# Kernel tuning notes

Hardware: AMD Instinct MI355X
Metric: run time of the kernel (lower is better)

The kernel has to match this reference:

```python
import jax, jax.numpy as jnp
import numpy as np

ALPHA = 16.0
K = 32
NUM_INSTANCES = 8  # samples per class in the batch (required by the original reshape logic)


def setup_inputs() -> dict:
    key = jax.random.key(0)
    n, d = 4096, 128
    inputs = jax.random.normal(key, (n, d), dtype=jnp.float32)
    # identity-sampler style labels: each class appears exactly NUM_INSTANCES times,
    # as assumed by the original pos_dist.resize(...) logic
    targets = (jnp.arange(n) // NUM_INSTANCES).astype(jnp.int64)
    return {"inputs": inputs, "targets": targets}


def reference(inputs, targets):
    n = inputs.shape[0]
    # L2-normalize rows (normalized=True)
    x = inputs / jnp.linalg.norm(inputs, axis=1, keepdims=True)
    # squared euclidean distance matrix: ||xi||^2 + ||xj||^2 - 2 xi.xj
    sq = jnp.sum(x * x, axis=1)  # [n]
    dist = sq[:, None] + sq[None, :] - 2.0 * (x @ x.T)  # [n, n]

    eye = jnp.eye(n, dtype=bool)
    same = targets[:, None] == targets[None, :]
    pos_mask = same & ~eye          # positives, excluding self
    neg_mask = ~same                # negatives

    inf = jnp.float32(jnp.inf)
    # threshold = K-th smallest (0-indexed) among the n-1 off-diagonal dists per row
    row_sorted = jnp.sort(jnp.where(eye, inf, dist), axis=1)
    thr = row_sorted[:, K]  # [n]

    base = jnp.mean(dist, axis=1, keepdims=True)  # mean over full row (incl. diagonal 0)
    below = dist < thr[:, None]
    pos_sel = pos_mask & below
    neg_sel = neg_mask & below

    expo = jnp.exp(ALPHA * (base - dist))  # [n, n]
    pos_logit = jnp.sum(jnp.where(pos_sel, expo, 0.0), axis=1)
    neg_logit = jnp.sum(jnp.where(neg_sel, expo, 0.0), axis=1)

    # fallback when no positive is below the threshold: use the closest positive
    min_pos = jnp.min(jnp.where(pos_mask, dist, inf), axis=1)
    fallback = jnp.exp(ALPHA * (base[:, 0] - min_pos))
    has_pos = jnp.any(pos_sel, axis=1)
    pos_logit = jnp.where(has_pos, pos_logit, fallback)

    loss_i = -jnp.log(pos_logit / (pos_logit + neg_logit))  # [n]
    loss = jnp.mean(loss_i)
    accuracy = jnp.mean((loss_i < 0.6).astype(jnp.float32))
    pos_d = jnp.sum(jnp.where(pos_mask, dist, 0.0)) / jnp.sum(pos_mask)
    neg_d = jnp.sum(jnp.where(neg_mask, dist, 0.0)) / jnp.sum(neg_mask)
    return loss, accuracy, pos_d, neg_d
```

## Files before the change

### kernel.cpp

```cpp
#include <hip/hip_runtime.h>
#include <math.h>

#define N 4096
#define D 128
#define RPB 8
#define NT 512
#define KSEL 32
#define CAND 320
#define ALPHA_C 16.0f

__device__ inline float waveSumF(float v){
  #pragma unroll
  for (int o = 32; o; o >>= 1) v += __shfl_xor(v, o);
  return v;
}
__device__ inline int waveSumI(int v){
  #pragma unroll
  for (int o = 32; o; o >>= 1) v += __shfl_xor(v, o);
  return v;
}
__device__ inline float waveMinF(float v){
  #pragma unroll
  for (int o = 32; o; o >>= 1) v = fminf(v, __shfl_xor(v, o));
  return v;
}

__device__ inline unsigned fkey(float f){
  unsigned u = __float_as_uint(f);
  return u ^ ((u >> 31) ? 0xFFFFFFFFu : 0x80000000u);
}
__device__ inline float fkey_inv(unsigned u){
  unsigned bits = (u & 0x80000000u) ? (u ^ 0x80000000u) : ~u;
  return __uint_as_float(bits);
}

__global__ __launch_bounds__(256) void knorm(const float* __restrict__ in,
                                             float* __restrict__ xn,
                                             float* __restrict__ xnT,
                                             float* __restrict__ sq){
  int row = blockIdx.x * 4 + (threadIdx.x >> 6);
  int lane = threadIdx.x & 63;
  const float* p = in + (size_t)row * D;
  float e0 = p[lane], e1 = p[lane + 64];
  float s = waveSumF(e0*e0 + e1*e1);
  float inv = 1.0f / sqrtf(s);
  float x0 = e0 * inv, x1 = e1 * inv;
  float s2 = waveSumF(x0*x0 + x1*x1);
  xn[(size_t)row * D + lane]      = x0;
  xn[(size_t)row * D + lane + 64] = x1;
  xnT[(size_t)lane * N + row]        = x0;
  xnT[(size_t)(lane + 64) * N + row] = x1;
  if (lane == 0) sq[row] = s2;
}

__global__ __launch_bounds__(NT, 2) void kmain(const float* __restrict__ xn,
                                               const float* __restrict__ xnT,
                                               const float* __restrict__ sq,
                                               const int* __restrict__ tgt,
                                               double* __restrict__ accum){
  __shared__ float dist[RPB][N];
  __shared__ float xi[RPB][D];
  __shared__ float cand[RPB][CAND];
  __shared__ int   ccnt[RPB];
  __shared__ float scr2[8][RPB + 2];
  __shared__ float scr3[8][RPB];
  __shared__ float baseSh[RPB], minposSh[RPB], lsSh[RPB], acSh[RPB];

  const int tid  = threadIdx.x;
  const int lane = tid & 63;
  const int w    = tid >> 6;
  const int i0   = blockIdx.x * RPB;

  for (int t = tid; t < RPB * D; t += NT)
    (&xi[0][0])[t] = xn[(size_t)i0 * D + t];
  if (tid < RPB) ccnt[tid] = 0;
  __syncthreads();

  float sqi[RPB]; int ti[RPB];
  #pragma unroll
  for (int r = 0; r < RPB; ++r){ sqi[r] = sq[i0 + r]; ti[r] = tgt[i0 + r]; }

  const int jA = 512 * w + 4 * lane;
  const int jB = jA + 256;
  const float4* T4 = (const float4*)xnT;
  const int fA = 128 * w + lane;
  const int fB = fA + 64;

  float acc[RPB][8];
  #pragma unroll
  for (int r = 0; r < RPB; ++r)
    #pragma unroll
    for (int q = 0; q < 8; ++q) acc[r][q] = 0.f;

  for (int k = 0; k < D; ++k){
    float4 vA = T4[(size_t)k * (N/4) + fA];
    float4 vB = T4[(size_t)k * (N/4) + fB];
    float xik[RPB];
    #pragma unroll
    for (int r = 0; r < RPB; ++r) xik[r] = xi[r][k];
    #pragma unroll
    for (int r = 0; r < RPB; ++r){
      acc[r][0] += xik[r] * vA.x;  acc[r][1] += xik[r] * vA.y;
      acc[r][2] += xik[r] * vA.z;  acc[r][3] += xik[r] * vA.w;
      acc[r][4] += xik[r] * vB.x;  acc[r][5] += xik[r] * vB.y;
      acc[r][6] += xik[r] * vB.z;  acc[r][7] += xik[r] * vB.w;
    }
  }

  float4 sqA = ((const float4*)sq)[fA], sqB = ((const float4*)sq)[fB];
  int4   tgA = ((const int4*)tgt)[fA],  tgB = ((const int4*)tgt)[fB];
  float sqj[8] = {sqA.x,sqA.y,sqA.z,sqA.w, sqB.x,sqB.y,sqB.z,sqB.w};
  int   tj [8] = {tgA.x,tgA.y,tgA.z,tgA.w, tgB.x,tgB.y,tgB.z,tgB.w};

  float bsum[RPB], mpos[RPB];
  #pragma unroll
  for (int r = 0; r < RPB; ++r){ bsum[r] = 0.f; mpos[r] = INFINITY; }
  float posd = 0.f, negd = 0.f;

  #pragma unroll
  for (int r = 0; r < RPB; ++r){
    float dv[8];
    #pragma unroll
    for (int q = 0; q < 8; ++q){
      int j = (q < 4) ? (jA + q) : (jB + q - 4);
      float dj = sqi[r] + sqj[q] - 2.0f * acc[r][q];
      bsum[r] += dj;
      bool same = (tj[q] == ti[r]);
      bool diag = (j == i0 + r);
      if (same && !diag){ posd += dj; mpos[r] = fminf(mpos[r], dj); }
      if (!same) negd += dj;
      dv[q] = diag ? INFINITY : dj;
    }
    ((float4*)&dist[r][jA])[0] = make_float4(dv[0], dv[1], dv[2], dv[3]);
    ((float4*)&dist[r][jB])[0] = make_float4(dv[4], dv[5], dv[6], dv[7]);
  }

  #pragma unroll
  for (int r = 0; r < RPB; ++r){
    float v = waveSumF(bsum[r]); if (lane == 0) scr2[w][r] = v;
    float m = waveMinF(mpos[r]); if (lane == 0) scr3[w][r] = m;
  }
  { float v = waveSumF(posd); if (lane == 0) scr2[w][RPB]   = v; }
  { float v = waveSumF(negd); if (lane == 0) scr2[w][RPB+1] = v; }
  __syncthreads();
  if (tid < RPB){
    float s = 0.f, m = INFINITY;
    #pragma unroll
    for (int q = 0; q < 8; ++q){ s += scr2[q][tid]; m = fminf(m, scr3[q][tid]); }
    baseSh[tid]   = s * (1.0f / (float)N);
    minposSh[tid] = m;
  }
  if (tid == RPB){
    float s = 0.f;
    #pragma unroll
    for (int q = 0; q < 8; ++q) s += scr2[q][RPB];
    atomicAdd(&accum[2], (double)s);
  }
  if (tid == RPB + 1){
    float s = 0.f;
    #pragma unroll
    for (int q = 0; q < 8; ++q) s += scr2[q][RPB+1];
    atomicAdd(&accum[3], (double)s);
  }
  __syncthreads();

  {
    const float4* drow = (const float4*)dist[w];
    unsigned lo = fkey(-0.5f);
    unsigned hi = fkey(4.5f);
    float thr;
    int   c = 0;
    bool  collected = false;

    while (hi - lo > 1u){
      unsigned mid = lo + ((hi - lo) >> 1);
      float pv = fkey_inv(mid);
      int cc = 0;
      #pragma unroll
      for (int t = 0; t < 16; ++t){
        float4 v = drow[lane + 64*t];
        cc += (v.x < pv) + (v.y < pv) + (v.z < pv) + (v.w < pv);
      }
      cc = waveSumI(cc);
      if (cc < KSEL + 1) lo = mid;
      else { hi = mid; if (cc <= CAND){ collected = true; c = cc; break; } }
    }

    if (collected){
      float pv = fkey_inv(hi);
      #pragma unroll
      for (int t = 0; t < 16; ++t){
        float4 v = drow[lane + 64*t];
        if (v.x < pv){ int ix = atomicAdd(&ccnt[w],1); if (ix < CAND) cand[w][ix] = v.x; }
        if (v.y < pv){ int ix = atomicAdd(&ccnt[w],1); if (ix < CAND) cand[w][ix] = v.y; }
        if (v.z < pv){ int ix = atomicAdd(&ccnt[w],1); if (ix < CAND) cand[w][ix] = v.z; }
        if (v.w < pv){ int ix = atomicAdd(&ccnt[w],1); if (ix < CAND) cand[w][ix] = v.w; }
      }
      __threadfence_block();
      float my[5]; int nm = 0;
      for (int t = lane; t < c; t += 64) my[nm++] = cand[w][t];
      for (int m = 0; m < nm; ++m){
        int myidx = lane + 64*m;
        float v = my[m];
        int rank = 0;
        for (int q = 0; q < c; ++q){
          float cq = cand[w][q];
          rank += (cq < v) || (cq == v && q < myidx);
        }
        if (rank == KSEL) lsSh[w] = v;
      }
      __threadfence_block();
      thr = lsSh[w];
    } else {
      thr = fkey_inv(lo);
    }

    const float base = baseSh[w];
    const int   tw   = ti[w];
    float pls = 0.f, nls = 0.f; int pcnt = 0;
    #pragma unroll 4
    for (int t = 0; t < 16; ++t){
      float4 v = drow[lane + 64*t];
      int4 tg = ((const int4*)tgt)[lane + 64*t];
      if (v.x < thr){ float e = expf(ALPHA_C*(base - v.x)); if (tg.x == tw){ pls += e; pcnt++; } else nls += e; }
      if (v.y < thr){ float e = expf(ALPHA_C*(base - v.y)); if (tg.y == tw){ pls += e; pcnt++; } else nls += e; }
      if (v.z < thr){ float e = expf(ALPHA_C*(base - v.z)); if (tg.z == tw){ pls += e; pcnt++; } else nls += e; }
      if (v.w < thr){ float e = expf(ALPHA_C*(base - v.w)); if (tg.w == tw){ pls += e; pcnt++; } else nls += e; }
    }
    pls = waveSumF(pls); nls = waveSumF(nls); pcnt = waveSumI(pcnt);
    if (lane == 0){
      float plogit = (pcnt > 0) ? pls : expf(ALPHA_C*(base - minposSh[w]));
      float li = -logf(plogit / (plogit + nls));
      lsSh[w] = li;
      acSh[w] = (li < 0.6f) ? 1.f : 0.f;
    }
  }
  __syncthreads();
  if (tid == 0){
    float ls = 0.f, ac = 0.f;
    #pragma unroll
    for (int r = 0; r < RPB; ++r){ ls += lsSh[r]; ac += acSh[r]; }
    atomicAdd(&accum[0], (double)ls);
    atomicAdd(&accum[1], (double)ac);
  }
}

__global__ void kfinal(const double* __restrict__ accum, float* __restrict__ out){
  out[0] = (float)(accum[0] / (double)N);
  out[1] = (float)(accum[1] / (double)N);
  out[2] = (float)(accum[2] / ((double)N * 7.0));
  out[3] = (float)(accum[3] / ((double)N * (double)(N - 8)));
}

extern "C" void kernel_launch(void* const* d_in, const int* in_sizes, int n_in,
                              void* d_out, int out_size, void* d_ws, size_t ws_size,
                              hipStream_t stream){
  (void)in_sizes; (void)n_in; (void)out_size; (void)ws_size;
  const float* in  = (const float*)d_in[0];
  const int*   tgt = (const int*)d_in[1];
  float* out = (float*)d_out;

  float*  xn    = (float*)d_ws;
  float*  xnT   = xn  + (size_t)N * D;
  float*  sq    = xnT + (size_t)N * D;
  double* accum = (double*)(sq + N);

  hipMemsetAsync(accum, 0, 4 * sizeof(double), stream);
  knorm <<<N/4, 256, 0, stream>>>(in, xn, xnT, sq);
  kmain <<<N/RPB, NT, 0, stream>>>(xn, xnT, sq, tgt, accum);
  kfinal<<<1, 1, 0, stream>>>(accum, out);
}
```

Baseline: 195.6 us.

## Keep distance rows in registers, drop shared dist buffer, fuse final reduction

Replaces the 128KB shared distance matrix with a small double-buffered shared staging area, so each wave ends up holding its full row (64 values per lane) in registers, and raises launch bounds to 4 blocks per CU. The threshold bisection now starts from the row minimum and splits on value midpoints, with a smaller candidate buffer. The memset and the final kernel are removed: accumulators are zeroed inside the normalize kernel and the last block writes the outputs via an atomic counter. The aim is higher occupancy and fewer launches, at the cost of 16 block-wide barriers during the transpose and heavy register pressure from the 64-float array.

```diff
diff --git a/kernel.cpp b/kernel.cpp
--- a/kernel.cpp
+++ b/kernel.cpp
@@ -6,7 +6,7 @@
 #define RPB 8
 #define NT 512
 #define KSEL 32
-#define CAND 320
+#define CAND 192
 #define ALPHA_C 16.0f
 
 __device__ inline float waveSumF(float v){
@@ -24,7 +24,6 @@
   for (int o = 32; o; o >>= 1) v = fminf(v, __shfl_xor(v, o));
   return v;
 }
-
 __device__ inline unsigned fkey(float f){
   unsigned u = __float_as_uint(f);
   return u ^ ((u >> 31) ? 0xFFFFFFFFu : 0x80000000u);
@@ -37,7 +36,13 @@
 __global__ __launch_bounds__(256) void knorm(const float* __restrict__ in,
                                              float* __restrict__ xn,
                                              float* __restrict__ xnT,
-                                             float* __restrict__ sq){
+                                             float* __restrict__ sq,
+                                             double* __restrict__ accum,
+                                             unsigned* __restrict__ ctr){
+  if (blockIdx.x == 0 && threadIdx.x < 8){
+    if (threadIdx.x < 4) accum[threadIdx.x] = 0.0;
+    if (threadIdx.x == 4) *ctr = 0u;
+  }
   int row = blockIdx.x * 4 + (threadIdx.x >> 6);
   int lane = threadIdx.x & 63;
   const float* p = in + (size_t)row * D;
@@ -53,18 +58,20 @@
   if (lane == 0) sq[row] = s2;
 }
 
-__global__ __launch_bounds__(NT, 2) void kmain(const float* __restrict__ xn,
+__global__ __launch_bounds__(NT, 4) void kmain(const float* __restrict__ xn,
                                                const float* __restrict__ xnT,
                                                const float* __restrict__ sq,
                                                const int* __restrict__ tgt,
-                                               double* __restrict__ accum){
-  __shared__ float dist[RPB][N];
+                                               double* __restrict__ accum,
+                                               unsigned* __restrict__ ctr,
+                                               float* __restrict__ out){
   __shared__ float xi[RPB][D];
+  __shared__ float buf[2][RPB][512];
   __shared__ float cand[RPB][CAND];
   __shared__ int   ccnt[RPB];
-  __shared__ float scr2[8][RPB + 2];
-  __shared__ float scr3[8][RPB];
-  __shared__ float baseSh[RPB], minposSh[RPB], lsSh[RPB], acSh[RPB];
+  __shared__ float scrB[RPB][RPB];
+  __shared__ float scrM[RPB][RPB];
+  __shared__ float scrP[RPB], scrN[RPB], lsSh[RPB], acSh[RPB];
 
   const int tid  = threadIdx.x;
   const int lane = tid & 63;
@@ -73,18 +80,16 @@
 
   for (int t = tid; t < RPB * D; t += NT)
     (&xi[0][0])[t] = xn[(size_t)i0 * D + t];
-  if (tid < RPB) ccnt[tid] = 0;
+  if (lane == 0){
+    ccnt[w] = 0;
+    #pragma unroll
+    for (int t = 0; t < RPB; ++t){ scrB[w][t] = 0.f; scrM[w][t] = INFINITY; }
+  }
   __syncthreads();
 
-  float sqi[RPB]; int ti[RPB];
-  #pragma unroll
-  for (int r = 0; r < RPB; ++r){ sqi[r] = sq[i0 + r]; ti[r] = tgt[i0 + r]; }
-
-  const int jA = 512 * w + 4 * lane;
-  const int jB = jA + 256;
-  const float4* T4 = (const float4*)xnT;
   const int fA = 128 * w + lane;
   const int fB = fA + 64;
+  const float4* T4 = (const float4*)xnT;
 
   float acc[RPB][8];
   #pragma unroll
@@ -107,129 +112,137 @@
     }
   }
 
-  float4 sqA = ((const float4*)sq)[fA], sqB = ((const float4*)sq)[fB];
-  int4   tgA = ((const int4*)tgt)[fA],  tgB = ((const int4*)tgt)[fB];
-  float sqj[8] = {sqA.x,sqA.y,sqA.z,sqA.w, sqB.x,sqB.y,sqB.z,sqB.w};
-  int   tj [8] = {tgA.x,tgA.y,tgA.z,tgA.w, tgB.x,tgB.y,tgB.z,tgB.w};
-
-  float bsum[RPB], mpos[RPB];
-  #pragma unroll
-  for (int r = 0; r < RPB; ++r){ bsum[r] = 0.f; mpos[r] = INFINITY; }
+  float d[64];
   float posd = 0.f, negd = 0.f;
 
   #pragma unroll
-  for (int r = 0; r < RPB; ++r){
-    float dv[8];
-    #pragma unroll
-    for (int q = 0; q < 8; ++q){
-      int j = (q < 4) ? (jA + q) : (jB + q - 4);
-      float dj = sqi[r] + sqj[q] - 2.0f * acc[r][q];
-      bsum[r] += dj;
-      bool same = (tj[q] == ti[r]);
-      bool diag = (j == i0 + r);
-      if (same && !diag){ posd += dj; mpos[r] = fminf(mpos[r], dj); }
+  for (int rr = 0; rr < 16; ++rr){
+    const int h = rr >> 3, t = rr & 7, A = rr & 1;
+    const float sqi_t = sq[i0 + t];
+    const int   ti_t  = tgt[i0 + t];
+    const int f = 128 * w + 64 * h + lane;
+    const float4 sq4 = ((const float4*)sq)[f];
+    const int4   tg4 = ((const int4*)tgt)[f];
+    const int jbase = 4 * f;
+    float dv[4]; float pb = 0.f, pm = INFINITY;
+    #pragma unroll
+    for (int q = 0; q < 4; ++q){
+      float sqjq = (q==0)?sq4.x:(q==1)?sq4.y:(q==2)?sq4.z:sq4.w;
+      int   tjq  = (q==0)?tg4.x:(q==1)?tg4.y:(q==2)?tg4.z:tg4.w;
+      float dj = sqi_t + sqjq - 2.0f * acc[t][h*4 + q];
+      pb += dj;
+      bool same = (tjq == ti_t);
+      bool diag = (jbase + q == i0 + t);
+      if (same && !diag){ posd += dj; pm = fminf(pm, dj); }
       if (!same) negd += dj;
       dv[q] = diag ? INFINITY : dj;
     }
-    ((float4*)&dist[r][jA])[0] = make_float4(dv[0], dv[1], dv[2], dv[3]);
-    ((float4*)&dist[r][jB])[0] = make_float4(dv[4], dv[5], dv[6], dv[7]);
-  }
-
-  #pragma unroll
-  for (int r = 0; r < RPB; ++r){
-    float v = waveSumF(bsum[r]); if (lane == 0) scr2[w][r] = v;
-    float m = waveMinF(mpos[r]); if (lane == 0) scr3[w][r] = m;
-  }
-  { float v = waveSumF(posd); if (lane == 0) scr2[w][RPB]   = v; }
-  { float v = waveSumF(negd); if (lane == 0) scr2[w][RPB+1] = v; }
+    float rb = waveSumF(pb);
+    float rm = waveMinF(pm);
+    if (lane == 0){ scrB[w][t] += rb; scrM[w][t] = fminf(scrM[w][t], rm); }
+    ((float4*)&buf[A][w][4*lane])[0] = make_float4(dv[0], dv[1], dv[2], dv[3]);
+    __syncthreads();
+    if (w == t){
+      #pragma unroll
+      for (int wp = 0; wp < 8; ++wp){
+        float4 v = ((const float4*)&buf[A][wp][4*lane])[0];
+        d[4*(2*wp + h) + 0] = v.x;  d[4*(2*wp + h) + 1] = v.y;
+        d[4*(2*wp + h) + 2] = v.z;  d[4*(2*wp + h) + 3] = v.w;
+      }
+    }
+  }
+
+  { float v = waveSumF(posd); if (lane == 0) scrP[w] = v; }
+  { float v = waveSumF(negd); if (lane == 0) scrN[w] = v; }
   __syncthreads();
-  if (tid < RPB){
-    float s = 0.f, m = INFINITY;
-    #pragma unroll
-    for (int q = 0; q < 8; ++q){ s += scr2[q][tid]; m = fminf(m, scr3[q][tid]); }
-    baseSh[tid]   = s * (1.0f / (float)N);
-    minposSh[tid] = m;
-  }
-  if (tid == RPB){
-    float s = 0.f;
-    #pragma unroll
-    for (int q = 0; q < 8; ++q) s += scr2[q][RPB];
-    atomicAdd(&accum[2], (double)s);
-  }
-  if (tid == RPB + 1){
-    float s = 0.f;
-    #pragma unroll
-    for (int q = 0; q < 8; ++q) s += scr2[q][RPB+1];
-    atomicAdd(&accum[3], (double)s);
-  }
-  __syncthreads();
-
+
+  float base, minpos;
   {
-    const float4* drow = (const float4*)dist[w];
-    unsigned lo = fkey(-0.5f);
+    float bp = (lane < 8) ? scrB[lane][w] : 0.f;
+    base = waveSumF(bp) * (1.0f / (float)N);
+    float mp = (lane < 8) ? scrM[lane][w] : INFINITY;
+    minpos = waveMinF(mp);
+  }
+  if (tid == 0){
+    double sp = 0.0, sn = 0.0;
+    #pragma unroll
+    for (int r = 0; r < RPB; ++r){ sp += (double)scrP[r]; sn += (double)scrN[r]; }
+    atomicAdd(&accum[2], sp);
+    atomicAdd(&accum[3], sn);
+  }
+
+  float thr;
+  {
+    float dmin = INFINITY;
+    #pragma unroll
+    for (int s = 0; s < 64; ++s) dmin = fminf(dmin, d[s]);
+    dmin = waveMinF(dmin);
+
+    unsigned lo = fkey(dmin);
     unsigned hi = fkey(4.5f);
-    float thr;
-    int   c = 0;
-    bool  collected = false;
+    int c = 0; bool have = false; float pvx = 0.f;
 
     while (hi - lo > 1u){
-      unsigned mid = lo + ((hi - lo) >> 1);
+      float loV = fkey_inv(lo), hiV = fkey_inv(hi);
+      unsigned mid = fkey(0.5f * (loV + hiV));
+      mid = (mid <= lo) ? lo + 1u : ((mid >= hi) ? hi - 1u : mid);
       float pv = fkey_inv(mid);
       int cc = 0;
       #pragma unroll
-      for (int t = 0; t < 16; ++t){
-        float4 v = drow[lane + 64*t];
-        cc += (v.x < pv) + (v.y < pv) + (v.z < pv) + (v.w < pv);
-      }
+      for (int s = 0; s < 64; ++s) cc += (d[s] < pv) ? 1 : 0;
       cc = waveSumI(cc);
       if (cc < KSEL + 1) lo = mid;
-      else { hi = mid; if (cc <= CAND){ collected = true; c = cc; break; } }
-    }
-
-    if (collected){
-      float pv = fkey_inv(hi);
-      #pragma unroll
-      for (int t = 0; t < 16; ++t){
-        float4 v = drow[lane + 64*t];
-        if (v.x < pv){ int ix = atomicAdd(&ccnt[w],1); if (ix < CAND) cand[w][ix] = v.x; }
-        if (v.y < pv){ int ix = atomicAdd(&ccnt[w],1); if (ix < CAND) cand[w][ix] = v.y; }
-        if (v.z < pv){ int ix = atomicAdd(&ccnt[w],1); if (ix < CAND) cand[w][ix] = v.z; }
-        if (v.w < pv){ int ix = atomicAdd(&ccnt[w],1); if (ix < CAND) cand[w][ix] = v.w; }
+      else { hi = mid; if (cc <= CAND){ c = cc; have = true; pvx = pv; break; } }
+    }
+
+    if (have){
+      #pragma unroll
+      for (int s = 0; s < 64; ++s){
+        if (d[s] < pvx){
+          int ix = atomicAdd(&ccnt[w], 1);
+          if (ix < CAND) cand[w][ix] = d[s];
+        }
       }
       __threadfence_block();
-      float my[5]; int nm = 0;
-      for (int t = lane; t < c; t += 64) my[nm++] = cand[w][t];
-      for (int m = 0; m < nm; ++m){
-        int myidx = lane + 64*m;
-        float v = my[m];
-        int rank = 0;
-        for (int q = 0; q < c; ++q){
-          float cq = cand[w][q];
-          rank += (cq < v) || (cq == v && q < myidx);
+      #pragma unroll
+      for (int m = 0; m < 3; ++m){
+        int idx = lane + 64 * m;
+        if (idx < c){
+          float v = cand[w][idx];
+          int rank = 0;
+          for (int q2 = 0; q2 < c; ++q2){
+            float cq = cand[w][q2];
+            rank += (cq < v) || (cq == v && q2 < idx);
+          }
+          if (rank == KSEL) lsSh[w] = v;
         }
-        if (rank == KSEL) lsSh[w] = v;
       }
       __threadfence_block();
       thr = lsSh[w];
     } else {
       thr = fkey_inv(lo);
     }
-
-    const float base = baseSh[w];
-    const int   tw   = ti[w];
+  }
+
+  {
+    const int tw = tgt[i0 + w];
     float pls = 0.f, nls = 0.f; int pcnt = 0;
-    #pragma unroll 4
-    for (int t = 0; t < 16; ++t){
-      float4 v = drow[lane + 64*t];
-      int4 tg = ((const int4*)tgt)[lane + 64*t];
-      if (v.x < thr){ float e = expf(ALPHA_C*(base - v.x)); if (tg.x == tw){ pls += e; pcnt++; } else nls += e; }
-      if (v.y < thr){ float e = expf(ALPHA_C*(base - v.y)); if (tg.y == tw){ pls += e; pcnt++; } else nls += e; }
-      if (v.z < thr){ float e = expf(ALPHA_C*(base - v.z)); if (tg.z == tw){ pls += e; pcnt++; } else nls += e; }
-      if (v.w < thr){ float e = expf(ALPHA_C*(base - v.w)); if (tg.w == tw){ pls += e; pcnt++; } else nls += e; }
+    #pragma unroll
+    for (int u = 0; u < 16; ++u){
+      int4 tg = ((const int4*)tgt)[64 * u + lane];
+      #pragma unroll
+      for (int q = 0; q < 4; ++q){
+        float dvq = d[4*u + q];
+        int   tjq = (q==0)?tg.x:(q==1)?tg.y:(q==2)?tg.z:tg.w;
+        if (dvq < thr){
+          float e = expf(ALPHA_C * (base - dvq));
+          if (tjq == tw){ pls += e; pcnt++; } else nls += e;
+        }
+      }
     }
     pls = waveSumF(pls); nls = waveSumF(nls); pcnt = waveSumI(pcnt);
     if (lane == 0){
-      float plogit = (pcnt > 0) ? pls : expf(ALPHA_C*(base - minposSh[w]));
+      float plogit = (pcnt > 0) ? pls : expf(ALPHA_C * (base - minpos));
       float li = -logf(plogit / (plogit + nls));
       lsSh[w] = li;
       acSh[w] = (li < 0.6f) ? 1.f : 0.f;
@@ -242,14 +255,19 @@
     for (int r = 0; r < RPB; ++r){ ls += lsSh[r]; ac += acSh[r]; }
     atomicAdd(&accum[0], (double)ls);
     atomicAdd(&accum[1], (double)ac);
-  }
-}
-
-__global__ void kfinal(const double* __restrict__ accum, float* __restrict__ out){
-  out[0] = (float)(accum[0] / (double)N);
-  out[1] = (float)(accum[1] / (double)N);
-  out[2] = (float)(accum[2] / ((double)N * 7.0));
-  out[3] = (float)(accum[3] / ((double)N * (double)(N - 8)));
+    __threadfence();
+    unsigned done = atomicAdd(ctr, 1u);
+    if (done == gridDim.x - 1){
+      double a0 = atomicAdd(&accum[0], 0.0);
+      double a1 = atomicAdd(&accum[1], 0.0);
+      double a2 = atomicAdd(&accum[2], 0.0);
+      double a3 = atomicAdd(&accum[3], 0.0);
+      out[0] = (float)(a0 / (double)N);
+      out[1] = (float)(a1 / (double)N);
+      out[2] = (float)(a2 / ((double)N * 7.0));
+      out[3] = (float)(a3 / ((double)N * (double)(N - 8)));
+    }
+  }
 }
 
 extern "C" void kernel_launch(void* const* d_in, const int* in_sizes, int n_in,
@@ -260,13 +278,12 @@
   const int*   tgt = (const int*)d_in[1];
   float* out = (float*)d_out;
 
-  float*  xn    = (float*)d_ws;
-  float*  xnT   = xn  + (size_t)N * D;
-  float*  sq    = xnT + (size_t)N * D;
-  double* accum = (double*)(sq + N);
-
-  hipMemsetAsync(accum, 0, 4 * sizeof(double), stream);
-  knorm <<<N/4, 256, 0, stream>>>(in, xn, xnT, sq);
-  kmain <<<N/RPB, NT, 0, stream>>>(xn, xnT, sq, tgt, accum);
-  kfinal<<<1, 1, 0, stream>>>(accum, out);
-}
+  float*    xn    = (float*)d_ws;
+  float*    xnT   = xn  + (size_t)N * D;
+  float*    sq    = xnT + (size_t)N * D;
+  double*   accum = (double*)(sq + N);
+  unsigned* ctr   = (unsigned*)(accum + 4);
+
+  knorm <<<N/4, 256, 0, stream>>>(in, xn, xnT, sq, accum, ctr);
+  kmain <<<N/RPB, NT, 0, stream>>>(xn, xnT, sq, tgt, accum, ctr, out);
+}
```

Result: no change. 194.0 us (-0.9%).
